# Kernel tuning notes

Hardware: AMD Instinct MI355X
Metric: run time of the kernel (lower is better)

The kernel has to match this reference:

```python
import jax, jax.numpy as jnp
import numpy as np
import math

H = 16
D_MODEL = 1024
D_K = D_MODEL // H
B, S = 4, 2048
NEG = -1.0e9


def setup_inputs() -> dict:
    key = jax.random.key(0)
    ks = jax.random.split(key, 13)
    scale = 1.0 / math.sqrt(D_MODEL)
    inp = {
        "query": jax.random.normal(ks[0], (B, S, D_MODEL), jnp.float32),
        "key": jax.random.normal(ks[1], (B, S, D_MODEL), jnp.float32),
        "value": jax.random.normal(ks[2], (B, S, D_MODEL), jnp.float32),
        "mask": jax.random.randint(ks[3], (B, S), 0, 2, jnp.int32),
        "Wq": jax.random.normal(ks[4], (D_MODEL, D_MODEL), jnp.float32) * scale,
        "bq": jax.random.normal(ks[5], (D_MODEL,), jnp.float32) * scale,
        "Wk": jax.random.normal(ks[6], (D_MODEL, D_MODEL), jnp.float32) * scale,
        "bk": jax.random.normal(ks[7], (D_MODEL,), jnp.float32) * scale,
        "Wv": jax.random.normal(ks[8], (D_MODEL, D_MODEL), jnp.float32) * scale,
        "bv": jax.random.normal(ks[9], (D_MODEL,), jnp.float32) * scale,
        "Wo": jax.random.normal(ks[10], (D_MODEL, D_MODEL), jnp.float32) * scale,
        "bo": jax.random.normal(ks[11], (D_MODEL,), jnp.float32) * scale,
    }
    return inp


def _split_heads(x):
    # [B, S, D] -> [B, H, S, D_K]
    b, s, _ = x.shape
    return x.reshape(b, s, H, D_K).transpose(0, 2, 1, 3)


def reference(query, key, value, mask, Wq, bq, Wk, bk, Wv, bv, Wo, bo):
    # torch nn.Linear: y = x @ W.T + b
    q = _split_heads(query @ Wq.T + bq)
    k = _split_heads(key @ Wk.T + bk)
    v = _split_heads(value @ Wv.T + bv)
    scores = jnp.einsum("bhqd,bhkd->bhqk", q, k) / math.sqrt(D_K)
    # [B, S] key-padding mask -> broadcast as [B, 1, 1, S] (== torch's [B,1,S,S] repeat)
    m = mask[:, None, None, :]
    scores = jnp.where(m == 0, NEG, scores)
    p = jax.nn.softmax(scores, axis=-1)
    out = jnp.einsum("bhqk,bhkd->bhqd", p, v)  # [B, H, S, D_K]
    out = out.transpose(0, 2, 1, 3).reshape(query.shape[0], -1, D_MODEL)
    return out @ Wo.T + bo
```

## Files before the change

### kernel.cpp

```cpp
#include <hip/hip_runtime.h>


#define DMODEL 1024
#define SLEN 2048
#define NHEAD 16
#define LOG2E 1.44269504088896340736f

typedef __attribute__((ext_vector_type(4))) float f32x4;
typedef __attribute__((ext_vector_type(8))) short bf16x8;
typedef __attribute__((ext_vector_type(4))) int i32x4;
typedef __attribute__((ext_vector_type(2))) int i32x2;

__device__ __forceinline__ unsigned short f2bf(float f) {
  __bf16 h = (__bf16)f;
  union { __bf16 h; unsigned short u; } cv; cv.h = h; return cv.u;
}
__device__ __forceinline__ unsigned pk(float a, float b) {
  return (unsigned)f2bf(a) | ((unsigned)f2bf(b) << 16);
}
__device__ __forceinline__ float fexp2(float x) {
  float r;
  asm("v_exp_f32 %0, %1" : "=v"(r) : "v"(x));
  return r;
}
__device__ __forceinline__ f32x4 zero4() {
  f32x4 z; z[0] = 0.f; z[1] = 0.f; z[2] = 0.f; z[3] = 0.f; return z;
}
__device__ __forceinline__ void gload16(const void* g, void* l) {
  __builtin_amdgcn_global_load_lds(
      (const __attribute__((address_space(1))) unsigned int*)(uintptr_t)g,
      (__attribute__((address_space(3))) unsigned int*)(uintptr_t)l, 16, 0, 0);
}

__global__ __launch_bounds__(256)
void cvt_pre(const float* __restrict__ xq, const float* __restrict__ xk,
             const float* __restrict__ xv,
             const float* __restrict__ Wq, const float* __restrict__ Wk,
             const float* __restrict__ Wv, const float* __restrict__ Wo,
             unsigned short* __restrict__ xbf, unsigned short* __restrict__ wbf,
             int full)
{
  const long nchunk = full ? 3670016L : 393216L;
  const long stride = (long)gridDim.x * blockDim.x;
  for (long c = (long)blockIdx.x * blockDim.x + threadIdx.x; c < nchunk; c += stride) {
    const float* src; unsigned short* dst; long off;
    if (full) {
      if (c < 3145728L) {
        const int i = (int)(c >> 20);
        off = (c & 1048575L) * 8;
        src = (i == 0) ? xq : (i == 1) ? xk : xv;
        dst = xbf + (size_t)i * 8388608;
      } else {
        const long d = c - 3145728L;
        const int j = (int)(d >> 17);
        off = (d & 131071L) * 8;
        src = (j == 0) ? Wq : (j == 1) ? Wk : (j == 2) ? Wv : Wo;
        dst = wbf + (size_t)j * 1048576;
      }
    } else {
      const int j = (int)(c >> 17);
      off = (c & 131071L) * 8;
      src = (j == 0) ? Wq : (j == 1) ? Wk : Wv;
      dst = wbf + (size_t)j * 1048576;
    }
    const float4 a = *(const float4*)(src + off);
    const float4 b = *(const float4*)(src + off + 4);
    i32x4 o;
    o[0] = (int)pk(a.x, a.y); o[1] = (int)pk(a.z, a.w);
    o[2] = (int)pk(b.x, b.y); o[3] = (int)pk(b.z, b.w);
    *(i32x4*)(dst + off) = o;
  }
}

template <bool ADMA>
__global__ __launch_bounds__(256)
void gemm_qkv_t(const float* __restrict__ xq, const float* __restrict__ xk,
                const float* __restrict__ xv,
                const unsigned short* __restrict__ xbf,
                const unsigned short* __restrict__ wbf,
                const float* __restrict__ bq, const float* __restrict__ bk,
                const float* __restrict__ bv,
                unsigned short* __restrict__ qw, unsigned short* __restrict__ kw,
                unsigned short* __restrict__ vw)
{
  const int bid = blockIdx.x;
  const int wg = (bid & 7) * 192 + (bid >> 3);
  const int z = wg >> 9;
  const int r = wg & 511;
  const int m0 = (r >> 3) * 128;
  const int n0 = (r & 7) * 128;

  const float* __restrict__ X = (z == 0) ? xq : (z == 1) ? xk : xv;
  const unsigned short* __restrict__ Xb = xbf + (size_t)z * 8388608;
  const unsigned short* __restrict__ Wb = wbf + (size_t)z * 1048576;
  const float* __restrict__ bias = (z == 0) ? bq : (z == 1) ? bk : bv;
  const float scale = (z == 0) ? 0.125f * LOG2E : 1.0f;

  const int tid = threadIdx.x;
  const int lane = tid & 63, wid = tid >> 6;
  const int l15 = lane & 15, g = lane >> 4;
  const int wr = wid >> 1, wc = wid & 1;

  __shared__ __align__(16) char LDS[32768];
  unsigned short* TT = (unsigned short*)LDS;

  auto dmaB = [&](int kt2, int bufsel) {
    char* dst = LDS + 16384 + bufsel * 8192;
#pragma unroll
    for (int q = 0; q < 2; ++q) {
      const int r0 = wid * 32 + q * 16;
      const unsigned short* src = Wb + (size_t)(n0 + r0 + (lane >> 2)) * 1024
                                     + kt2 * 32 + (lane & 3) * 8;
      gload16(src, dst + r0 * 64);
    }
  };
  auto dmaA = [&](int kt2, int bufsel) {
    char* dst = LDS + bufsel * 8192;
#pragma unroll
    for (int q = 0; q < 2; ++q) {
      const int r0 = wid * 32 + q * 16;
      const unsigned short* src = Xb + (size_t)(m0 + r0 + (lane >> 2)) * 1024
                                     + kt2 * 32 + (lane & 3) * 8;
      gload16(src, dst + r0 * 64);
    }
  };

  const int srow = tid >> 1, sh = tid & 1;
  const float* __restrict__ Ag = X + (size_t)(m0 + srow) * DMODEL + sh * 16;
  const unsigned sw0 = (unsigned)(srow * 64) + (((unsigned)(sh * 2))     ^ ((unsigned)((srow >> 1) & 3))) * 16;
  const unsigned sw1 = (unsigned)(srow * 64) + (((unsigned)(sh * 2 + 1)) ^ ((unsigned)((srow >> 1) & 3))) * 16;
  f32x4 ar4[4];
  auto loadA = [&](int kt2) {
    const float* p = Ag + kt2 * 32;
#pragma unroll
    for (int j = 0; j < 4; ++j) ar4[j] = *(const f32x4*)(p + j * 4);
  };
  auto packA = [&](int bufsel) {
    char* Ab = LDS + bufsel * 8192;
    i32x4 wv0, wv1;
    wv0[0] = (int)pk(ar4[0][0], ar4[0][1]); wv0[1] = (int)pk(ar4[0][2], ar4[0][3]);
    wv0[2] = (int)pk(ar4[1][0], ar4[1][1]); wv0[3] = (int)pk(ar4[1][2], ar4[1][3]);
    wv1[0] = (int)pk(ar4[2][0], ar4[2][1]); wv1[1] = (int)pk(ar4[2][2], ar4[2][3]);
    wv1[2] = (int)pk(ar4[3][0], ar4[3][1]); wv1[3] = (int)pk(ar4[3][2], ar4[3][3]);
    *(i32x4*)(Ab + sw0) = wv0;
    *(i32x4*)(Ab + sw1) = wv1;
  };

  f32x4 acc[4][4];
#pragma unroll
  for (int i = 0; i < 4; ++i)
#pragma unroll
    for (int j = 0; j < 4; ++j) acc[i][j] = zero4();

  if (ADMA) {
    dmaA(0, 0);
  } else {
    loadA(0); packA(0); loadA(1);
  }
  dmaB(0, 0);
  __syncthreads();

  for (int kt = 0; kt < 32; ++kt) {
    const int cur = kt & 1;
    if (kt + 1 < 32) {
      dmaB(kt + 1, cur ^ 1);
      if (ADMA) dmaA(kt + 1, cur ^ 1);
      else      packA(cur ^ 1);
    }
    if (!ADMA && kt + 2 < 32) loadA(kt + 2);

    const char* Ab = LDS + cur * 8192;
    const char* Bb = LDS + 16384 + cur * 8192;
    bf16x8 afr[4], bfr[4];
#pragma unroll
    for (int i = 0; i < 4; ++i) {
      const int ra = wr * 64 + i * 16 + l15;
      const unsigned ab = ADMA ? (unsigned)(g * 16)
                               : ((unsigned)(g ^ ((ra >> 1) & 3)) * 16);
      afr[i] = *(const bf16x8*)(Ab + ra * 64 + ab);
      const int rb = wc * 64 + i * 16 + l15;
      bfr[i] = *(const bf16x8*)(Bb + rb * 64 + g * 16);
    }
#pragma unroll
    for (int mi = 0; mi < 4; ++mi)
#pragma unroll
      for (int ni = 0; ni < 4; ++ni)
        acc[mi][ni] = __builtin_amdgcn_mfma_f32_16x16x32_bf16(
            afr[mi], bfr[ni], acc[mi][ni], 0, 0, 0);

    if (kt + 1 < 32) __syncthreads();
  }

  float bv4[4];
#pragma unroll
  for (int ni = 0; ni < 4; ++ni) bv4[ni] = bias[n0 + wc * 64 + ni * 16 + l15];

  if (z == 2) {
    const int bb = m0 >> 11, s0 = m0 & 2047;
#pragma unroll
    for (int p = 0; p < 2; ++p) {
      __syncthreads();
      if (wc == p) {
#pragma unroll
        for (int mi = 0; mi < 4; ++mi)
#pragma unroll
          for (int ni = 0; ni < 4; ++ni)
#pragma unroll
            for (int rr2 = 0; rr2 < 4; ++rr2)
              TT[(ni * 16 + l15) * 136 + wr * 64 + mi * 16 + 4 * g + rr2] =
                  f2bf(acc[mi][ni][rr2] + bv4[ni]);
      }
      __syncthreads();
      const int rr = tid >> 2, cc = (tid & 3) * 32;
      unsigned short* dp = vw + ((size_t)(bb * 1024 + n0 + p * 64 + rr)) * 2048 + s0 + cc;
      const unsigned short* sp = &TT[rr * 136 + cc];
#pragma unroll
      for (int j = 0; j < 4; ++j)
        *(i32x4*)(void*)(dp + j * 8) = *(const i32x4*)(const void*)(sp + j * 8);
    }
    return;
  }

  unsigned short* __restrict__ dst = (z == 0) ? qw : kw;
#pragma unroll
  for (int mi = 0; mi < 4; ++mi) {
#pragma unroll
    for (int ni = 0; ni < 4; ++ni) {
      const int n = n0 + wc * 64 + ni * 16 + l15;
      const int h = n >> 6, d = n & 63;
#pragma unroll
      for (int rr2 = 0; rr2 < 4; ++rr2) {
        const int m = m0 + wr * 64 + mi * 16 + 4 * g + rr2;
        const int b = m >> 11, s = m & 2047;
        const float val = (acc[mi][ni][rr2] + bv4[ni]) * scale;
        dst[((size_t)(b * NHEAD + h) * SLEN + s) * 64 + d] = f2bf(val);
      }
    }
  }
}

__global__ __launch_bounds__(256, 3)
void attn(const unsigned short* __restrict__ q_ws,
          const unsigned short* __restrict__ k_ws,
          const unsigned short* __restrict__ vT,
          const int* __restrict__ mask,
          unsigned short* __restrict__ o_ws)
{
  const int bh = blockIdx.x;
  const int qt = blockIdx.y;
  const int b = bh >> 4, h = bh & 15;
  const int tid = threadIdx.x, w = tid >> 6, lane = tid & 63;
  const int l15 = lane & 15, g = lane >> 4;

  __shared__ __align__(16) unsigned short Kb[2][64 * 64];
  __shared__ __align__(16) unsigned short Vb[2][64 * 64];
  __shared__ __align__(16) unsigned short Pl[4][16 * 64];

  const int* __restrict__ maskp = mask + b * SLEN;

  const size_t head = (size_t)bh * SLEN;
  const int r8 = lane >> 3, c8 = lane & 7;
  const int swz = ((c8 ^ r8) * 16);
  const unsigned pswz = (unsigned)((l15 & 7) << 4);

  const int qbase = qt * 128 + w * 32;
  bf16x8 qf[2][2];
  {
    const unsigned short* qp0 = q_ws + (head + qbase + l15) * 64;
    const unsigned short* qp1 = q_ws + (head + qbase + 16 + l15) * 64;
    qf[0][0] = *(const bf16x8*)(qp0 + g * 8);
    qf[0][1] = *(const bf16x8*)(qp0 + 32 + g * 8);
    qf[1][0] = *(const bf16x8*)(qp1 + g * 8);
    qf[1][1] = *(const bf16x8*)(qp1 + 32 + g * 8);
  }

  auto stage = [&](int kt2, int bufi) {
#pragma unroll
    for (int cl = 0; cl < 2; ++cl) {
      const int rr = w * 16 + cl * 8 + r8;
      const char* gk = (const char*)(k_ws + (head + kt2 * 64 + rr) * 64) + swz;
      gload16(gk, &Kb[bufi][(w * 16 + cl * 8) * 64]);
      const char* gv = (const char*)(vT + ((size_t)(bh * 64 + rr)) * SLEN + kt2 * 64) + swz;
      gload16(gv, &Vb[bufi][(w * 16 + cl * 8) * 64]);
    }
  };

  stage(0, 0);
  __syncthreads();

  float m_run[2] = {-1e30f, -1e30f};
  float l_run[2] = {0.f, 0.f};
  f32x4 of[2][4];
#pragma unroll
  for (int qi = 0; qi < 2; ++qi)
#pragma unroll
    for (int n = 0; n < 4; ++n) of[qi][n] = zero4();

  unsigned short* Pw = (unsigned short*)Pl[w];
  int cur = 0;

  for (int kt = 0; kt < 32; ++kt) {
    const int kv0 = kt * 64;
    f32x4 mv[4];
#pragma unroll
    for (int s = 0; s < 4; ++s) {
      const int4 mm = *(const int4*)(maskp + kv0 + s * 16 + g * 4);
      mv[s][0] = mm.x ? 0.f : -1e9f;
      mv[s][1] = mm.y ? 0.f : -1e9f;
      mv[s][2] = mm.z ? 0.f : -1e9f;
      mv[s][3] = mm.w ? 0.f : -1e9f;
    }
    if (kt + 1 < 32) stage(kt + 1, cur ^ 1);
    const char* Kc = (const char*)Kb[cur];
    const char* Vc = (const char*)Vb[cur];

#pragma unroll
    for (int qi = 0; qi < 2; ++qi) {
      f32x4 sac[4];
      __builtin_amdgcn_s_setprio(1);
#pragma unroll
      for (int s = 0; s < 4; ++s) {
        const char* kr = Kc + (s * 16 + l15) * 128;
        const bf16x8 kf0 = *(const bf16x8*)(kr + ((unsigned)(g * 16) ^ pswz));
        const bf16x8 kf1 = *(const bf16x8*)(kr + ((unsigned)(64 + g * 16) ^ pswz));
        f32x4 zt = mv[s];
        zt = __builtin_amdgcn_mfma_f32_16x16x32_bf16(kf0, qf[qi][0], zt, 0, 0, 0);
        sac[s] = __builtin_amdgcn_mfma_f32_16x16x32_bf16(kf1, qf[qi][1], zt, 0, 0, 0);
      }
      __builtin_amdgcn_s_setprio(0);

      float tmax = -3.0e38f;
#pragma unroll
      for (int s = 0; s < 4; ++s)
#pragma unroll
        for (int rr = 0; rr < 4; ++rr) tmax = fmaxf(tmax, sac[s][rr]);
      tmax = fmaxf(tmax, __shfl_xor(tmax, 16));
      tmax = fmaxf(tmax, __shfl_xor(tmax, 32));
      if (!__all(tmax <= m_run[qi] + 8.f)) {
        const float mnew = fmaxf(m_run[qi], tmax);
        const float alpha = fexp2(m_run[qi] - mnew);
        float af[4];
#pragma unroll
        for (int rr = 0; rr < 4; ++rr) af[rr] = __shfl(alpha, g * 4 + rr);
#pragma unroll
        for (int n = 0; n < 4; ++n)
#pragma unroll
          for (int rr = 0; rr < 4; ++rr) of[qi][n][rr] *= af[rr];
        l_run[qi] *= alpha;
        m_run[qi] = mnew;
      }
      float psum = 0.f;
      unsigned pr[4][2];
#pragma unroll
      for (int s = 0; s < 4; ++s) {
        const float p0 = fexp2(sac[s][0] - m_run[qi]);
        const float p1 = fexp2(sac[s][1] - m_run[qi]);
        const float p2 = fexp2(sac[s][2] - m_run[qi]);
        const float p3 = fexp2(sac[s][3] - m_run[qi]);
        psum += (p0 + p1) + (p2 + p3);
        pr[s][0] = pk(p0, p1); pr[s][1] = pk(p2, p3);
      }
      l_run[qi] += psum;
#pragma unroll
      for (int s = 0; s < 4; ++s) {
        i32x2 wv; wv[0] = (int)pr[s][0]; wv[1] = (int)pr[s][1];
        *(i32x2*)(void*)((char*)Pw + l15 * 128 + ((unsigned)(s * 32 + g * 8) ^ pswz)) = wv;
      }

      __builtin_amdgcn_s_setprio(1);
#pragma unroll
      for (int k2 = 0; k2 < 2; ++k2) {
        const bf16x8 pa = *(const bf16x8*)(const void*)(
            (const char*)Pw + l15 * 128 + ((unsigned)(k2 * 64 + g * 16) ^ pswz));
#pragma unroll
        for (int n = 0; n < 4; ++n) {
          const bf16x8 vf = *(const bf16x8*)(
              Vc + (n * 16 + l15) * 128 + ((unsigned)(k2 * 64 + g * 16) ^ pswz));
          of[qi][n] = __builtin_amdgcn_mfma_f32_16x16x32_bf16(pa, vf, of[qi][n], 0, 0, 0);
        }
      }
      __builtin_amdgcn_s_setprio(0);
    }
    __syncthreads();
    cur ^= 1;
  }

#pragma unroll
  for (int qi = 0; qi < 2; ++qi) {
    float lt = l_run[qi];
    lt += __shfl_xor(lt, 16);
    lt += __shfl_xor(lt, 32);
    float inv[4];
#pragma unroll
    for (int rr = 0; rr < 4; ++rr) inv[rr] = 1.f / __shfl(lt, g * 4 + rr);
    const int qrow0 = qt * 128 + w * 32 + qi * 16;
#pragma unroll
    for (int n = 0; n < 4; ++n) {
      const int d = h * 64 + n * 16 + l15;
#pragma unroll
      for (int rr = 0; rr < 4; ++rr) {
        const int sr = qrow0 + 4 * g + rr;
        o_ws[((size_t)b * SLEN + sr) * DMODEL + d] = f2bf(of[qi][n][rr] * inv[rr]);
      }
    }
  }
}

template <bool DMA>
__global__ __launch_bounds__(256)
void gemm_out_t(const unsigned short* __restrict__ ow,
                const unsigned short* __restrict__ wob,
                const float* __restrict__ Wo, const float* __restrict__ bo,
                float* __restrict__ out)
{
  const int bid = blockIdx.x;
  const int wg = (bid & 7) * 64 + (bid >> 3);
  const int m0 = (wg >> 3) * 128;
  const int n0 = (wg & 7) * 128;

  const int tid = threadIdx.x;
  const int lane = tid & 63, wid = tid >> 6;
  const int l15 = lane & 15, g = lane >> 4;
  const int wr = wid >> 1, wc = wid & 1;

  __shared__ __align__(16) char LDS[32768];

  auto dmaA = [&](int kt2, int bufsel) {
    char* dst = LDS + bufsel * 8192;
#pragma unroll
    for (int q = 0; q < 2; ++q) {
      const int r0 = wid * 32 + q * 16;
      const unsigned short* src = ow + (size_t)(m0 + r0 + (lane >> 2)) * 1024
                                     + kt2 * 32 + (lane & 3) * 8;
      gload16(src, dst + r0 * 64);
    }
  };
  auto dmaB = [&](int kt2, int bufsel) {
    char* dst = LDS + 16384 + bufsel * 8192;
#pragma unroll
    for (int q = 0; q < 2; ++q) {
      const int r0 = wid * 32 + q * 16;
      const unsigned short* src = wob + (size_t)(n0 + r0 + (lane >> 2)) * 1024
                                      + kt2 * 32 + (lane & 3) * 8;
      gload16(src, dst + r0 * 64);
    }
  };

  const int srow = tid >> 1, sh = tid & 1;
  const unsigned short* __restrict__ Ag = ow + (size_t)(m0 + srow) * DMODEL + sh * 16;
  const float* __restrict__ Bg = Wo + (size_t)(n0 + srow) * DMODEL + sh * 16;
  const unsigned sw0 = (unsigned)(srow * 64) + (((unsigned)(sh * 2))     ^ ((unsigned)((srow >> 1) & 3))) * 16;
  const unsigned sw1 = (unsigned)(srow * 64) + (((unsigned)(sh * 2 + 1)) ^ ((unsigned)((srow >> 1) & 3))) * 16;
  i32x4 ar2[2];
  f32x4 br4[4];
  auto loadA = [&](int kt2) {
    const unsigned short* p = Ag + kt2 * 32;
    ar2[0] = *(const i32x4*)(p);
    ar2[1] = *(const i32x4*)(p + 8);
  };
  auto loadB = [&](int kt2) {
    const float* p = Bg + kt2 * 32;
#pragma unroll
    for (int j = 0; j < 4; ++j) br4[j] = *(const f32x4*)(p + j * 4);
  };
  auto packA = [&](int bufsel) {
    char* Ab = LDS + bufsel * 8192;
    *(i32x4*)(Ab + sw0) = ar2[0];
    *(i32x4*)(Ab + sw1) = ar2[1];
  };
  auto packB = [&](int bufsel) {
    char* Bb = LDS + 16384 + bufsel * 8192;
    i32x4 wv0, wv1;
    wv0[0] = (int)pk(br4[0][0], br4[0][1]); wv0[1] = (int)pk(br4[0][2], br4[0][3]);
    wv0[2] = (int)pk(br4[1][0], br4[1][1]); wv0[3] = (int)pk(br4[1][2], br4[1][3]);
    wv1[0] = (int)pk(br4[2][0], br4[2][1]); wv1[1] = (int)pk(br4[2][2], br4[2][3]);
    wv1[2] = (int)pk(br4[3][0], br4[3][1]); wv1[3] = (int)pk(br4[3][2], br4[3][3]);
    *(i32x4*)(Bb + sw0) = wv0;
    *(i32x4*)(Bb + sw1) = wv1;
  };

  f32x4 acc[4][4];
#pragma unroll
  for (int i = 0; i < 4; ++i)
#pragma unroll
    for (int j = 0; j < 4; ++j) acc[i][j] = zero4();

  if (DMA) {
    dmaA(0, 0); dmaB(0, 0);
  } else {
    loadA(0); loadB(0);
    packA(0); packB(0);
    loadA(1); loadB(1);
  }
  __syncthreads();

  for (int kt = 0; kt < 32; ++kt) {
    const int cur = kt & 1;
    if (kt + 1 < 32) {
      if (DMA) { dmaA(kt + 1, cur ^ 1); dmaB(kt + 1, cur ^ 1); }
      else     { packA(cur ^ 1); packB(cur ^ 1); }
    }
    if (!DMA && kt + 2 < 32) { loadA(kt + 2); loadB(kt + 2); }

    const char* Ab = LDS + cur * 8192;
    const char* Bb = LDS + 16384 + cur * 8192;
    bf16x8 afr[4], bfr[4];
#pragma unroll
    for (int i = 0; i < 4; ++i) {
      const int ra = wr * 64 + i * 16 + l15;
      const unsigned ab = DMA ? (unsigned)(g * 16)
                              : ((unsigned)(g ^ ((ra >> 1) & 3)) * 16);
      afr[i] = *(const bf16x8*)(Ab + ra * 64 + ab);
      const int rb = wc * 64 + i * 16 + l15;
      const unsigned bb2 = DMA ? (unsigned)(g * 16)
                               : ((unsigned)(g ^ ((rb >> 1) & 3)) * 16);
      bfr[i] = *(const bf16x8*)(Bb + rb * 64 + bb2);
    }
#pragma unroll
    for (int mi = 0; mi < 4; ++mi)
#pragma unroll
      for (int ni = 0; ni < 4; ++ni)
        acc[mi][ni] = __builtin_amdgcn_mfma_f32_16x16x32_bf16(
            afr[mi], bfr[ni], acc[mi][ni], 0, 0, 0);

    if (kt + 1 < 32) __syncthreads();
  }

  float bv4[4];
#pragma unroll
  for (int ni = 0; ni < 4; ++ni) bv4[ni] = bo[n0 + wc * 64 + ni * 16 + l15];
#pragma unroll
  for (int mi = 0; mi < 4; ++mi) {
#pragma unroll
    for (int ni = 0; ni < 4; ++ni) {
      const int n = n0 + wc * 64 + ni * 16 + l15;
#pragma unroll
      for (int rr = 0; rr < 4; ++rr) {
        const int m = m0 + wr * 64 + mi * 16 + 4 * g + rr;
        out[(size_t)m * DMODEL + n] = acc[mi][ni][rr] + bv4[ni];
      }
    }
  }
}

extern "C" void kernel_launch(void* const* d_in, const int* in_sizes, int n_in,
                              void* d_out, int out_size, void* d_ws, size_t ws_size,
                              hipStream_t stream) {
  const float* query = (const float*)d_in[0];
  const float* key_  = (const float*)d_in[1];
  const float* value = (const float*)d_in[2];
  const int*   mask  = (const int*)d_in[3];
  const float* Wq = (const float*)d_in[4];
  const float* bq = (const float*)d_in[5];
  const float* Wk = (const float*)d_in[6];
  const float* bk = (const float*)d_in[7];
  const float* Wv = (const float*)d_in[8];
  const float* bv = (const float*)d_in[9];
  const float* Wo = (const float*)d_in[10];
  const float* bo = (const float*)d_in[11];
  float* out = (float*)d_out;

  const size_t MiB = 1048576;
  char* ws = (char*)d_ws;
  unsigned short* q_ws = (unsigned short*)(ws);
  unsigned short* k_ws = (unsigned short*)(ws + 16 * MiB);
  unsigned short* vT   = (unsigned short*)(ws + 32 * MiB);
  unsigned short* o_ws = (unsigned short*)(ws + 48 * MiB);

  const bool big = ws_size >= 120 * MiB;
  unsigned short* xbf = big ? (unsigned short*)(ws + 64 * MiB) : (unsigned short*)0;
  unsigned short* wbf = big ? (unsigned short*)(ws + 112 * MiB)
                            : (unsigned short*)(ws + 48 * MiB);

  cvt_pre<<<dim3(2048), 256, 0, stream>>>(query, key_, value, Wq, Wk, Wv, Wo,
                                          xbf, wbf, big ? 1 : 0);
  if (big)
    gemm_qkv_t<true><<<dim3(1536), 256, 0, stream>>>(query, key_, value, xbf, wbf,
                                                     bq, bk, bv, q_ws, k_ws, vT);
  else
    gemm_qkv_t<false><<<dim3(1536), 256, 0, stream>>>(query, key_, value, xbf, wbf,
                                                      bq, bk, bv, q_ws, k_ws, vT);
  attn<<<dim3(64, 16), 256, 0, stream>>>(q_ws, k_ws, vT, mask, o_ws);
  if (big)
    gemm_out_t<true><<<dim3(512), 256, 0, stream>>>(o_ws, wbf + (size_t)3 * 1048576,
                                                    Wo, bo, out);
  else
    gemm_out_t<false><<<dim3(512), 256, 0, stream>>>(o_ws, (const unsigned short*)0,
                                                     Wo, bo, out);
}
```

Baseline: 259.4 us.

## Shrink attention tiles to 64 queries and 32 keys for higher occupancy

The attention kernel now gives each wave 16 query rows instead of 32 and streams K/V in 32-key tiles instead of 64, with the shared-memory swizzles rewritten to fit. The grid doubles along the query axis and the launch bound asks for 8 blocks per CU instead of 3. The aim is more resident waves and more blocks to hide latency and spread the softmax work. In exchange, K/V tiles are loaded from global memory twice as often overall, and each step does less MFMA work per barrier and per softmax rescale check.

```diff
diff --git a/kernel.cpp b/kernel.cpp
--- a/kernel.cpp
+++ b/kernel.cpp
@@ -239,7 +239,7 @@
   }
 }
 
-__global__ __launch_bounds__(256, 3)
+__global__ __launch_bounds__(256, 8)
 void attn(const unsigned short* __restrict__ q_ws,
           const unsigned short* __restrict__ k_ws,
           const unsigned short* __restrict__ vT,
@@ -252,156 +252,143 @@
   const int tid = threadIdx.x, w = tid >> 6, lane = tid & 63;
   const int l15 = lane & 15, g = lane >> 4;
 
-  __shared__ __align__(16) unsigned short Kb[2][64 * 64];
-  __shared__ __align__(16) unsigned short Vb[2][64 * 64];
-  __shared__ __align__(16) unsigned short Pl[4][16 * 64];
+  __shared__ __align__(16) unsigned short Kb[2][32 * 64];
+  __shared__ __align__(16) unsigned short Vb[2][64 * 32];
+  __shared__ __align__(16) unsigned short Pl[4][16 * 32];
 
   const int* __restrict__ maskp = mask + b * SLEN;
-
   const size_t head = (size_t)bh * SLEN;
+
   const int r8 = lane >> 3, c8 = lane & 7;
-  const int swz = ((c8 ^ r8) * 16);
-  const unsigned pswz = (unsigned)((l15 & 7) << 4);
-
-  const int qbase = qt * 128 + w * 32;
-  bf16x8 qf[2][2];
+  const int kswz = (c8 ^ r8) * 16;
+  const int r4 = lane >> 2, c4 = lane & 3;
+  const int vswz = (c4 ^ (r4 & 3)) * 16;
+
+  const unsigned pswzK = (unsigned)((l15 & 7) << 4);
+  const unsigned pswzV = (unsigned)((l15 & 3) << 4);
+
+  const int qbase = qt * 64 + w * 16;
+  bf16x8 qf0, qf1;
   {
-    const unsigned short* qp0 = q_ws + (head + qbase + l15) * 64;
-    const unsigned short* qp1 = q_ws + (head + qbase + 16 + l15) * 64;
-    qf[0][0] = *(const bf16x8*)(qp0 + g * 8);
-    qf[0][1] = *(const bf16x8*)(qp0 + 32 + g * 8);
-    qf[1][0] = *(const bf16x8*)(qp1 + g * 8);
-    qf[1][1] = *(const bf16x8*)(qp1 + 32 + g * 8);
+    const unsigned short* qp = q_ws + (head + qbase + l15) * 64;
+    qf0 = *(const bf16x8*)(qp + g * 8);
+    qf1 = *(const bf16x8*)(qp + 32 + g * 8);
   }
 
   auto stage = [&](int kt2, int bufi) {
-#pragma unroll
-    for (int cl = 0; cl < 2; ++cl) {
-      const int rr = w * 16 + cl * 8 + r8;
-      const char* gk = (const char*)(k_ws + (head + kt2 * 64 + rr) * 64) + swz;
-      gload16(gk, &Kb[bufi][(w * 16 + cl * 8) * 64]);
-      const char* gv = (const char*)(vT + ((size_t)(bh * 64 + rr)) * SLEN + kt2 * 64) + swz;
-      gload16(gv, &Vb[bufi][(w * 16 + cl * 8) * 64]);
-    }
+    const int kr = w * 8 + r8;
+    const char* gk = (const char*)(k_ws + (head + kt2 * 32 + kr) * 64) + kswz;
+    gload16(gk, &Kb[bufi][(w * 8) * 64]);
+    const int vr = w * 16 + r4;
+    const char* gv = (const char*)(vT + ((size_t)(bh * 64 + vr)) * SLEN + kt2 * 32) + vswz;
+    gload16(gv, &Vb[bufi][(w * 16) * 32]);
   };
 
   stage(0, 0);
   __syncthreads();
 
-  float m_run[2] = {-1e30f, -1e30f};
-  float l_run[2] = {0.f, 0.f};
-  f32x4 of[2][4];
-#pragma unroll
-  for (int qi = 0; qi < 2; ++qi)
-#pragma unroll
-    for (int n = 0; n < 4; ++n) of[qi][n] = zero4();
+  float m_run = -1e30f, l_run = 0.f;
+  f32x4 of[4];
+#pragma unroll
+  for (int n = 0; n < 4; ++n) of[n] = zero4();
 
   unsigned short* Pw = (unsigned short*)Pl[w];
   int cur = 0;
 
-  for (int kt = 0; kt < 32; ++kt) {
-    const int kv0 = kt * 64;
-    f32x4 mv[4];
-#pragma unroll
-    for (int s = 0; s < 4; ++s) {
+  for (int kt = 0; kt < 64; ++kt) {
+    const int kv0 = kt * 32;
+    f32x4 mv[2];
+#pragma unroll
+    for (int s = 0; s < 2; ++s) {
       const int4 mm = *(const int4*)(maskp + kv0 + s * 16 + g * 4);
       mv[s][0] = mm.x ? 0.f : -1e9f;
       mv[s][1] = mm.y ? 0.f : -1e9f;
       mv[s][2] = mm.z ? 0.f : -1e9f;
       mv[s][3] = mm.w ? 0.f : -1e9f;
     }
-    if (kt + 1 < 32) stage(kt + 1, cur ^ 1);
+    if (kt + 1 < 64) stage(kt + 1, cur ^ 1);
     const char* Kc = (const char*)Kb[cur];
     const char* Vc = (const char*)Vb[cur];
 
-#pragma unroll
-    for (int qi = 0; qi < 2; ++qi) {
-      f32x4 sac[4];
-      __builtin_amdgcn_s_setprio(1);
-#pragma unroll
-      for (int s = 0; s < 4; ++s) {
-        const char* kr = Kc + (s * 16 + l15) * 128;
-        const bf16x8 kf0 = *(const bf16x8*)(kr + ((unsigned)(g * 16) ^ pswz));
-        const bf16x8 kf1 = *(const bf16x8*)(kr + ((unsigned)(64 + g * 16) ^ pswz));
-        f32x4 zt = mv[s];
-        zt = __builtin_amdgcn_mfma_f32_16x16x32_bf16(kf0, qf[qi][0], zt, 0, 0, 0);
-        sac[s] = __builtin_amdgcn_mfma_f32_16x16x32_bf16(kf1, qf[qi][1], zt, 0, 0, 0);
-      }
-      __builtin_amdgcn_s_setprio(0);
-
-      float tmax = -3.0e38f;
-#pragma unroll
-      for (int s = 0; s < 4; ++s)
-#pragma unroll
-        for (int rr = 0; rr < 4; ++rr) tmax = fmaxf(tmax, sac[s][rr]);
-      tmax = fmaxf(tmax, __shfl_xor(tmax, 16));
-      tmax = fmaxf(tmax, __shfl_xor(tmax, 32));
-      if (!__all(tmax <= m_run[qi] + 8.f)) {
-        const float mnew = fmaxf(m_run[qi], tmax);
-        const float alpha = fexp2(m_run[qi] - mnew);
-        float af[4];
-#pragma unroll
-        for (int rr = 0; rr < 4; ++rr) af[rr] = __shfl(alpha, g * 4 + rr);
-#pragma unroll
-        for (int n = 0; n < 4; ++n)
-#pragma unroll
-          for (int rr = 0; rr < 4; ++rr) of[qi][n][rr] *= af[rr];
-        l_run[qi] *= alpha;
-        m_run[qi] = mnew;
-      }
-      float psum = 0.f;
-      unsigned pr[4][2];
-#pragma unroll
-      for (int s = 0; s < 4; ++s) {
-        const float p0 = fexp2(sac[s][0] - m_run[qi]);
-        const float p1 = fexp2(sac[s][1] - m_run[qi]);
-        const float p2 = fexp2(sac[s][2] - m_run[qi]);
-        const float p3 = fexp2(sac[s][3] - m_run[qi]);
-        psum += (p0 + p1) + (p2 + p3);
-        pr[s][0] = pk(p0, p1); pr[s][1] = pk(p2, p3);
-      }
-      l_run[qi] += psum;
-#pragma unroll
-      for (int s = 0; s < 4; ++s) {
-        i32x2 wv; wv[0] = (int)pr[s][0]; wv[1] = (int)pr[s][1];
-        *(i32x2*)(void*)((char*)Pw + l15 * 128 + ((unsigned)(s * 32 + g * 8) ^ pswz)) = wv;
-      }
-
-      __builtin_amdgcn_s_setprio(1);
-#pragma unroll
-      for (int k2 = 0; k2 < 2; ++k2) {
-        const bf16x8 pa = *(const bf16x8*)(const void*)(
-            (const char*)Pw + l15 * 128 + ((unsigned)(k2 * 64 + g * 16) ^ pswz));
-#pragma unroll
-        for (int n = 0; n < 4; ++n) {
-          const bf16x8 vf = *(const bf16x8*)(
-              Vc + (n * 16 + l15) * 128 + ((unsigned)(k2 * 64 + g * 16) ^ pswz));
-          of[qi][n] = __builtin_amdgcn_mfma_f32_16x16x32_bf16(pa, vf, of[qi][n], 0, 0, 0);
-        }
-      }
-      __builtin_amdgcn_s_setprio(0);
-    }
+    f32x4 sac[2];
+    __builtin_amdgcn_s_setprio(1);
+#pragma unroll
+    for (int s = 0; s < 2; ++s) {
+      const char* kr = Kc + (s * 16 + l15) * 128;
+      const bf16x8 kf0 = *(const bf16x8*)(kr + ((unsigned)(g * 16) ^ pswzK));
+      const bf16x8 kf1 = *(const bf16x8*)(kr + ((unsigned)(64 + g * 16) ^ pswzK));
+      f32x4 zt = mv[s];
+      zt = __builtin_amdgcn_mfma_f32_16x16x32_bf16(kf0, qf0, zt, 0, 0, 0);
+      sac[s] = __builtin_amdgcn_mfma_f32_16x16x32_bf16(kf1, qf1, zt, 0, 0, 0);
+    }
+    __builtin_amdgcn_s_setprio(0);
+
+    float tmax = -3.0e38f;
+#pragma unroll
+    for (int s = 0; s < 2; ++s)
+#pragma unroll
+      for (int rr = 0; rr < 4; ++rr) tmax = fmaxf(tmax, sac[s][rr]);
+    tmax = fmaxf(tmax, __shfl_xor(tmax, 16));
+    tmax = fmaxf(tmax, __shfl_xor(tmax, 32));
+    if (!__all(tmax <= m_run + 8.f)) {
+      const float mnew = fmaxf(m_run, tmax);
+      const float alpha = fexp2(m_run - mnew);
+      float af[4];
+#pragma unroll
+      for (int rr = 0; rr < 4; ++rr) af[rr] = __shfl(alpha, g * 4 + rr);
+#pragma unroll
+      for (int n = 0; n < 4; ++n)
+#pragma unroll
+        for (int rr = 0; rr < 4; ++rr) of[n][rr] *= af[rr];
+      l_run *= alpha;
+      m_run = mnew;
+    }
+    float psum = 0.f;
+    unsigned pr[2][2];
+#pragma unroll
+    for (int s = 0; s < 2; ++s) {
+      const float p0 = fexp2(sac[s][0] - m_run);
+      const float p1 = fexp2(sac[s][1] - m_run);
+      const float p2 = fexp2(sac[s][2] - m_run);
+      const float p3 = fexp2(sac[s][3] - m_run);
+      psum += (p0 + p1) + (p2 + p3);
+      pr[s][0] = pk(p0, p1); pr[s][1] = pk(p2, p3);
+    }
+    l_run += psum;
+#pragma unroll
+    for (int s = 0; s < 2; ++s) {
+      i32x2 wv; wv[0] = (int)pr[s][0]; wv[1] = (int)pr[s][1];
+      *(i32x2*)(void*)((char*)Pw + l15 * 64 + (((unsigned)(s * 32 + g * 8)) ^ pswzV)) = wv;
+    }
+
+    const bf16x8 pa = *(const bf16x8*)(const void*)(
+        (const char*)Pw + l15 * 64 + (((unsigned)(g * 16)) ^ pswzV));
+    __builtin_amdgcn_s_setprio(1);
+#pragma unroll
+    for (int n = 0; n < 4; ++n) {
+      const bf16x8 vf = *(const bf16x8*)(
+          Vc + (n * 16 + l15) * 64 + (((unsigned)(g * 16)) ^ pswzV));
+      of[n] = __builtin_amdgcn_mfma_f32_16x16x32_bf16(pa, vf, of[n], 0, 0, 0);
+    }
+    __builtin_amdgcn_s_setprio(0);
     __syncthreads();
     cur ^= 1;
   }
 
-#pragma unroll
-  for (int qi = 0; qi < 2; ++qi) {
-    float lt = l_run[qi];
-    lt += __shfl_xor(lt, 16);
-    lt += __shfl_xor(lt, 32);
-    float inv[4];
-#pragma unroll
-    for (int rr = 0; rr < 4; ++rr) inv[rr] = 1.f / __shfl(lt, g * 4 + rr);
-    const int qrow0 = qt * 128 + w * 32 + qi * 16;
-#pragma unroll
-    for (int n = 0; n < 4; ++n) {
-      const int d = h * 64 + n * 16 + l15;
-#pragma unroll
-      for (int rr = 0; rr < 4; ++rr) {
-        const int sr = qrow0 + 4 * g + rr;
-        o_ws[((size_t)b * SLEN + sr) * DMODEL + d] = f2bf(of[qi][n][rr] * inv[rr]);
-      }
+  float lt = l_run;
+  lt += __shfl_xor(lt, 16);
+  lt += __shfl_xor(lt, 32);
+  float inv[4];
+#pragma unroll
+  for (int rr = 0; rr < 4; ++rr) inv[rr] = 1.f / __shfl(lt, g * 4 + rr);
+  const int qrow0 = qt * 64 + w * 16;
+#pragma unroll
+  for (int n = 0; n < 4; ++n) {
+    const int d = h * 64 + n * 16 + l15;
+#pragma unroll
+    for (int rr = 0; rr < 4; ++rr) {
+      const int sr = qrow0 + 4 * g + rr;
+      o_ws[((size_t)b * SLEN + sr) * DMODEL + d] = f2bf(of[n][rr] * inv[rr]);
     }
   }
 }
@@ -580,7 +567,7 @@
   else
     gemm_qkv_t<false><<<dim3(1536), 256, 0, stream>>>(query, key_, value, xbf, wbf,
                                                       bq, bk, bv, q_ws, k_ws, vT);
-  attn<<<dim3(64, 16), 256, 0, stream>>>(q_ws, k_ws, vT, mask, o_ws);
+  attn<<<dim3(64, 32), 256, 0, stream>>>(q_ws, k_ws, vT, mask, o_ws);
   if (big)
     gemm_out_t<true><<<dim3(512), 256, 0, stream>>>(o_ws, wbf + (size_t)3 * 1048576,
                                                     Wo, bo, out);
```

New measurement: 283.8 us. +9.4%, slower.
